# Performance work log

Hardware: AMD Instinct MI355X
Metric: run time of the kernel (lower is better)

The kernel has to match this reference:

```python
import jax, jax.numpy as jnp
import numpy as np

D_HEAD = 64
KERNEL = 7


def make_neighbourhood_mask(kernel: int, ch: int, cw: int) -> jnp.ndarray:
    """Boolean mask [ch*cw, ch*cw]; True where key is inside the query's k x k window."""
    h_ramp = jnp.arange(ch)
    w_ramp = jnp.arange(cw)
    h_pos, w_pos = jnp.meshgrid(h_ramp, w_ramp, indexing='ij')  # [ch, cw]
    start_h = jnp.clip(h_pos - kernel // 2, 0, ch - kernel)[..., None, None]
    end_h = start_h + kernel
    start_w = jnp.clip(w_pos - kernel // 2, 0, cw - kernel)[..., None, None]
    end_w = start_w + kernel
    h_range = h_ramp.reshape(1, 1, ch, 1)
    w_range = w_ramp.reshape(1, 1, 1, cw)
    mask = (h_range >= start_h) & (h_range < end_h) & (w_range >= start_w) & (w_range < end_w)
    return mask.reshape(ch * cw, ch * cw)


def setup_inputs() -> dict:
    key = jax.random.key(0)
    k1, k2, k3 = jax.random.split(key, 3)
    B, H, W, D = 2, 64, 64, 384
    x = jax.random.normal(k1, (B, H, W, D), dtype=jnp.float32)
    w_qkv = jax.random.normal(k2, (3 * D, D), dtype=jnp.float32) * 0.02
    w_out = jax.random.normal(k3, (D, D), dtype=jnp.float32) * 0.02
    return {"x": x, "w_qkv": w_qkv, "w_out": w_out}


def reference(x, w_qkv, w_out):
    B, H, W, D = x.shape
    nh = D // D_HEAD
    N = H * W
    # qkv projection: Linear(D, 3D, bias=False) -> x @ w_qkv.T
    qkv = jnp.einsum('bhwd,ed->bhwe', x, w_qkv)  # [B,H,W,3D]
    # 'n h w (t nh e) -> t n nh (h w) e'
    qkv = qkv.reshape(B, N, 3, nh, D_HEAD)
    qkv = jnp.transpose(qkv, (2, 0, 3, 1, 4))  # [3, B, nh, N, e]
    q, k, v = qkv[0], qkv[1], qkv[2]
    mask = make_neighbourhood_mask(KERNEL, H, W)  # [N, N] bool
    scale = 1.0 / jnp.sqrt(jnp.asarray(D_HEAD, dtype=x.dtype))
    scores = jnp.einsum('bnqe,bnke->bnqk', q, k) * scale  # [B,nh,N,N]
    neg = jnp.asarray(jnp.finfo(scores.dtype).min, dtype=scores.dtype)
    scores = jnp.where(mask[None, None], scores, neg)
    attn = jax.nn.softmax(scores, axis=-1)
    out = jnp.einsum('bnqk,bnke->bnqe', attn, v)  # [B,nh,N,e]
    # 'n nh (h w) e -> n h w (nh e)'
    out = jnp.transpose(out, (0, 2, 1, 3)).reshape(B, H, W, D)
    return jnp.einsum('bhwd,ed->bhwe', out, w_out)
```

## Files before the change

kernel.cpp:

```cpp
#include <hip/hip_runtime.h>
#include <hip/hip_bf16.h>

typedef __attribute__((ext_vector_type(8))) short bf16x8;
typedef __attribute__((ext_vector_type(4))) short s16x4;
typedef __attribute__((ext_vector_type(4))) float fx4;

#define MFMA16(a, b, c) __builtin_amdgcn_mfma_f32_16x16x32_bf16((a), (b), (c), 0, 0, 0)

__device__ __forceinline__ short f2bf(float f) {
  unsigned u = __float_as_uint(f);
  u += 0x7fffu + ((u >> 16) & 1u);
  return (short)(u >> 16);
}

__device__ __forceinline__ void gl_lds16(const short* g, short* l) {
  __builtin_amdgcn_global_load_lds((const __attribute__((address_space(1))) void*)(g),
                                   (__attribute__((address_space(3))) void*)(l), 16, 0, 0);
}

__global__ __launch_bounds__(256) void convert_k(
    const float* __restrict__ x, const float* __restrict__ wq, const float* __restrict__ wo,
    short* __restrict__ xb, short* __restrict__ wb, short* __restrict__ wob) {
  const int i4 = (blockIdx.x * 256 + threadIdx.x) * 4;
  {
    float4 v = *(const float4*)(x + i4);
    s16x4 s; s[0] = f2bf(v.x); s[1] = f2bf(v.y); s[2] = f2bf(v.z); s[3] = f2bf(v.w);
    *(s16x4*)(xb + i4) = s;
  }
  if (i4 < 1152 * 384) {
    float4 v = *(const float4*)(wq + i4);
    s16x4 s; s[0] = f2bf(v.x); s[1] = f2bf(v.y); s[2] = f2bf(v.z); s[3] = f2bf(v.w);
    *(s16x4*)(wb + i4) = s;
  }
  if (i4 < 384 * 384) {
    float4 v = *(const float4*)(wo + i4);
    s16x4 s; s[0] = f2bf(v.x); s[1] = f2bf(v.y); s[2] = f2bf(v.z); s[3] = f2bf(v.w);
    *(s16x4*)(wob + i4) = s;
  }
}

__global__ __launch_bounds__(256) void qkv_gemm(
    const short* __restrict__ A, const short* __restrict__ Bw,
    short* __restrict__ qb, short* __restrict__ kb, short* __restrict__ vb) {
  __shared__ __align__(16) short As[128 * 32];
  __shared__ __align__(16) short Bs[128 * 32];
  const int mt = blockIdx.x / 9, nt = blockIdx.x % 9;
  const int m0 = mt * 128, n0 = nt * 128;
  const int tid = threadIdx.x;
  const int lane = tid & 63, w = tid >> 6;
  const int wr = w >> 1, wc = w & 1;
  const int l15 = lane & 15, l4 = lane >> 4;
  const int srow = lane >> 2, schunk = (lane & 3) * 8;
  const fx4 vzero = {0.f, 0.f, 0.f, 0.f};
  fx4 acc[4][4];
#pragma unroll
  for (int i = 0; i < 4; i++)
#pragma unroll
    for (int j = 0; j < 4; j++) acc[i][j] = vzero;

  for (int kt = 0; kt < 384; kt += 32) {
    __syncthreads();
    gl_lds16(A + (size_t)(m0 + w * 16 + srow) * 384 + kt + schunk, As + (w * 16) * 32);
    gl_lds16(A + (size_t)(m0 + 64 + w * 16 + srow) * 384 + kt + schunk, As + (64 + w * 16) * 32);
    gl_lds16(Bw + (size_t)(n0 + w * 16 + srow) * 384 + kt + schunk, Bs + (w * 16) * 32);
    gl_lds16(Bw + (size_t)(n0 + 64 + w * 16 + srow) * 384 + kt + schunk, Bs + (64 + w * 16) * 32);
    __syncthreads();
    bf16x8 af[4], bfr[4];
#pragma unroll
    for (int i = 0; i < 4; i++) {
      af[i]  = *(const bf16x8*)(As + (wr * 64 + i * 16 + l15) * 32 + l4 * 8);
      bfr[i] = *(const bf16x8*)(Bs + (wc * 64 + i * 16 + l15) * 32 + l4 * 8);
    }
#pragma unroll
    for (int i = 0; i < 4; i++)
#pragma unroll
      for (int j = 0; j < 4; j++)
        acc[i][j] = MFMA16(af[i], bfr[j], acc[i][j]);
  }
#pragma unroll
  for (int j = 0; j < 4; j++) {
    const int e = n0 + wc * 64 + j * 16 + l15;
    const int t = e / 384;
    const int rem = e - t * 384;
    const int head = rem >> 6, d = rem & 63;
    short* __restrict__ dst = (t == 0) ? qb : (t == 1) ? kb : vb;
#pragma unroll
    for (int i = 0; i < 4; i++) {
      const int mb = m0 + wr * 64 + i * 16 + l4 * 4;
#pragma unroll
      for (int r = 0; r < 4; r++) {
        const int m = mb + r;
        const int b = m >> 12, pix = m & 4095;
        dst[((b * 6 + head) * 4096 + pix) * 64 + d] = f2bf(acc[i][j][r]);
      }
    }
  }
}

__global__ __launch_bounds__(256) void natt_k(
    const short* __restrict__ qg, const short* __restrict__ kg, const short* __restrict__ vg,
    short* __restrict__ ob) {
  __shared__ __align__(16) short lds[30976];
  short* Ks = lds;
  short* Vt = lds + 16128;
  short* Ps = lds;

  const int bid = blockIdx.x;
  const int tile = bid & 63, bh = bid >> 6;
  const int h0 = (tile >> 3) * 8, w0 = (tile & 7) * 8;
  const int ph0 = max(h0 - 3, 0), pw0 = max(w0 - 3, 0);
  const int prows = min(h0 + 4, 57) + 7 - ph0;
  const int pcols = min(w0 + 4, 57) + 7 - pw0;
  const short* kb = kg + (size_t)bh * 4096 * 64;
  const short* vb = vg + (size_t)bh * 4096 * 64;
  const short* qb = qg + (size_t)bh * 4096 * 64;
  const int tid = threadIdx.x;

  for (int i = tid; i < 224 * 8; i += 256) {
    const int kk = i >> 3, dc = i & 7;
    const int kr = kk >> 4, kc = kk & 15;
    const int krc = min(kr, prows - 1), kcc = min(kc, pcols - 1);
    const int pix = (ph0 + krc) * 64 + (pw0 + kcc);
    *(bf16x8*)(Ks + kk * 72 + dc * 8) = *(const bf16x8*)(kb + pix * 64 + dc * 8);
    const bf16x8 vv = *(const bf16x8*)(vb + pix * 64 + dc * 8);
#pragma unroll
    for (int j = 0; j < 8; j++) Vt[(dc * 8 + j) * 232 + kk] = vv[j];
  }
  __syncthreads();

  const int lane = tid & 63, w = tid >> 6;
  const int l15 = lane & 15, l4 = lane >> 4;

  const int qa = w * 16 + l15;
  const int qpixa = (h0 + (qa >> 3)) * 64 + (w0 + (qa & 7));
  const bf16x8 aq0 = *(const bf16x8*)(qb + qpixa * 64 + l4 * 8);
  const bf16x8 aq1 = *(const bf16x8*)(qb + qpixa * 64 + 32 + l4 * 8);

  const fx4 vzero = {0.f, 0.f, 0.f, 0.f};
  fx4 s[14];
#pragma unroll
  for (int n = 0; n < 14; n++) s[n] = vzero;
#pragma unroll
  for (int n = 0; n < 14; n++) {
    const bf16x8 b0 = *(const bf16x8*)(Ks + (n * 16 + l15) * 72 + l4 * 8);
    const bf16x8 b1 = *(const bf16x8*)(Ks + (n * 16 + l15) * 72 + 32 + l4 * 8);
    s[n] = MFMA16(aq0, b0, s[n]);
    s[n] = MFMA16(aq1, b1, s[n]);
  }

#pragma unroll
  for (int r = 0; r < 4; r++) {
    const int q = w * 16 + l4 * 4 + r;
    const int qh = h0 + (q >> 3), qw = w0 + (q & 7);
    const int sh = min(max(qh - 3, 0), 57) - ph0;
    const int sw = min(max(qw - 3, 0), 57) - pw0;
    float m = -1e30f;
#pragma unroll
    for (int n = 0; n < 14; n++) {
      const bool valid = (n >= sh) && (n < sh + 7) && (l15 >= sw) && (l15 < sw + 7);
      const float val = valid ? s[n][r] * 0.125f : -1e30f;
      s[n][r] = val;
      m = fmaxf(m, val);
    }
    m = fmaxf(m, __shfl_xor(m, 1));
    m = fmaxf(m, __shfl_xor(m, 2));
    m = fmaxf(m, __shfl_xor(m, 4));
    m = fmaxf(m, __shfl_xor(m, 8));
    float sum = 0.f;
#pragma unroll
    for (int n = 0; n < 14; n++) {
      const float e = __expf(s[n][r] - m);
      s[n][r] = e;
      sum += e;
    }
    sum += __shfl_xor(sum, 1);
    sum += __shfl_xor(sum, 2);
    sum += __shfl_xor(sum, 4);
    sum += __shfl_xor(sum, 8);
    const float inv = 1.f / sum;
#pragma unroll
    for (int n = 0; n < 14; n++) s[n][r] *= inv;
  }

  __syncthreads();

#pragma unroll
  for (int n = 0; n < 14; n++)
#pragma unroll
    for (int r = 0; r < 4; r++)
      Ps[(w * 16 + l4 * 4 + r) * 232 + n * 16 + l15] = f2bf(s[n][r]);

  __syncthreads();

  fx4 o[4];
#pragma unroll
  for (int j = 0; j < 4; j++) o[j] = vzero;
#pragma unroll
  for (int ks = 0; ks < 7; ks++) {
    const bf16x8 pa = *(const bf16x8*)(Ps + (w * 16 + l15) * 232 + ks * 32 + l4 * 8);
#pragma unroll
    for (int j = 0; j < 4; j++) {
      const bf16x8 vf = *(const bf16x8*)(Vt + (j * 16 + l15) * 232 + ks * 32 + l4 * 8);
      o[j] = MFMA16(pa, vf, o[j]);
    }
  }

  const int b = bh / 6, head = bh % 6;
#pragma unroll
  for (int j = 0; j < 4; j++) {
    const int d = j * 16 + l15;
#pragma unroll
    for (int r = 0; r < 4; r++) {
      const int q = w * 16 + l4 * 4 + r;
      const int pix = (h0 + (q >> 3)) * 64 + (w0 + (q & 7));
      ob[(size_t)(b * 4096 + pix) * 384 + head * 64 + d] = f2bf(o[j][r]);
    }
  }
}

__global__ __launch_bounds__(256) void out_gemm(
    const short* __restrict__ A, const short* __restrict__ Bw, float* __restrict__ out) {
  __shared__ __align__(16) short As[64 * 32];
  __shared__ __align__(16) short Bs[128 * 32];
  const int mt = blockIdx.x / 3, nt = blockIdx.x % 3;
  const int m0 = mt * 64, n0 = nt * 128;
  const int tid = threadIdx.x;
  const int lane = tid & 63, w = tid >> 6;
  const int wr = w >> 1, wc = w & 1;
  const int l15 = lane & 15, l4 = lane >> 4;
  const int srow = lane >> 2, schunk = (lane & 3) * 8;
  const fx4 vzero = {0.f, 0.f, 0.f, 0.f};
  fx4 acc[2][4];
#pragma unroll
  for (int i = 0; i < 2; i++)
#pragma unroll
    for (int j = 0; j < 4; j++) acc[i][j] = vzero;

  for (int kt = 0; kt < 384; kt += 32) {
    __syncthreads();
    gl_lds16(A + (size_t)(m0 + w * 16 + srow) * 384 + kt + schunk, As + (w * 16) * 32);
    gl_lds16(Bw + (size_t)(n0 + w * 16 + srow) * 384 + kt + schunk, Bs + (w * 16) * 32);
    gl_lds16(Bw + (size_t)(n0 + 64 + w * 16 + srow) * 384 + kt + schunk, Bs + (64 + w * 16) * 32);
    __syncthreads();
    bf16x8 af[2], bfr[4];
#pragma unroll
    for (int i = 0; i < 2; i++)
      af[i]  = *(const bf16x8*)(As + (wr * 32 + i * 16 + l15) * 32 + l4 * 8);
#pragma unroll
    for (int j = 0; j < 4; j++)
      bfr[j] = *(const bf16x8*)(Bs + (wc * 64 + j * 16 + l15) * 32 + l4 * 8);
#pragma unroll
    for (int i = 0; i < 2; i++)
#pragma unroll
      for (int j = 0; j < 4; j++)
        acc[i][j] = MFMA16(af[i], bfr[j], acc[i][j]);
  }
#pragma unroll
  for (int j = 0; j < 4; j++) {
    const int e = n0 + wc * 64 + j * 16 + l15;
#pragma unroll
    for (int i = 0; i < 2; i++) {
      const int mb = m0 + wr * 32 + i * 16 + l4 * 4;
#pragma unroll
      for (int r = 0; r < 4; r++)
        out[(size_t)(mb + r) * 384 + e] = acc[i][j][r];
    }
  }
}

extern "C" void kernel_launch(void* const* d_in, const int* in_sizes, int n_in,
                              void* d_out, int out_size, void* d_ws, size_t ws_size,
                              hipStream_t stream) {
  const float* x  = (const float*)d_in[0];
  const float* wq = (const float*)d_in[1];
  const float* wo = (const float*)d_in[2];
  float* out = (float*)d_out;

  short* xb  = (short*)d_ws;
  short* wb  = xb + 8192 * 384;
  short* wob = wb + 1152 * 384;
  short* qb  = wob + 384 * 384;
  short* kb  = qb + 3145728;
  short* vb  = kb + 3145728;
  short* ob  = vb + 3145728;

  convert_k<<<3072, 256, 0, stream>>>(x, wq, wo, xb, wb, wob);
  qkv_gemm<<<576, 256, 0, stream>>>(xb, wb, qb, kb, vb);
  natt_k<<<768, 256, 0, stream>>>(qb, kb, vb, ob);
  out_gemm<<<384, 256, 0, stream>>>(ob, wob, out);
}
```

Baseline: 54.97 us.

## Widen GEMM K-tile to 64 with XOR-swizzled LDS, remap blocks across XCDs, restructure V transpose

Both GEMMs now stage 64-wide K slices per iteration instead of 32, halving barrier and loop overhead. An XOR swizzle on the LDS column chunk avoids bank conflicts on fragment reads. Block indices in all three kernels are permuted so consecutive tiles land on the same XCD, which should improve L2 locality. The attention kernel's V transpose moves to one thread per key row looping over all chunks, which changes the LDS write pattern and leaves 32 threads idle.

```diff
diff --git a/kernel.cpp b/kernel.cpp
--- a/kernel.cpp
+++ b/kernel.cpp
@@ -42,15 +42,17 @@
 __global__ __launch_bounds__(256) void qkv_gemm(
     const short* __restrict__ A, const short* __restrict__ Bw,
     short* __restrict__ qb, short* __restrict__ kb, short* __restrict__ vb) {
-  __shared__ __align__(16) short As[128 * 32];
-  __shared__ __align__(16) short Bs[128 * 32];
-  const int mt = blockIdx.x / 9, nt = blockIdx.x % 9;
+  __shared__ __align__(16) short As[128 * 64];
+  __shared__ __align__(16) short Bs[128 * 64];
+  const int orig = (blockIdx.x & 7) * 72 + (blockIdx.x >> 3);
+  const int mt = orig / 9, nt = orig % 9;
   const int m0 = mt * 128, n0 = nt * 128;
   const int tid = threadIdx.x;
   const int lane = tid & 63, w = tid >> 6;
   const int wr = w >> 1, wc = w & 1;
   const int l15 = lane & 15, l4 = lane >> 4;
-  const int srow = lane >> 2, schunk = (lane & 3) * 8;
+  const int srow = lane >> 3;
+  const int scol = ((lane & 7) ^ (srow & 7)) * 8;
   const fx4 vzero = {0.f, 0.f, 0.f, 0.f};
   fx4 acc[4][4];
 #pragma unroll
@@ -58,24 +60,32 @@
 #pragma unroll
     for (int j = 0; j < 4; j++) acc[i][j] = vzero;
 
-  for (int kt = 0; kt < 384; kt += 32) {
+  for (int kt = 0; kt < 384; kt += 64) {
     __syncthreads();
-    gl_lds16(A + (size_t)(m0 + w * 16 + srow) * 384 + kt + schunk, As + (w * 16) * 32);
-    gl_lds16(A + (size_t)(m0 + 64 + w * 16 + srow) * 384 + kt + schunk, As + (64 + w * 16) * 32);
-    gl_lds16(Bw + (size_t)(n0 + w * 16 + srow) * 384 + kt + schunk, Bs + (w * 16) * 32);
-    gl_lds16(Bw + (size_t)(n0 + 64 + w * 16 + srow) * 384 + kt + schunk, Bs + (64 + w * 16) * 32);
+#pragma unroll
+    for (int q = 0; q < 4; q++) {
+      gl_lds16(A  + (size_t)(m0 + w * 32 + q * 8 + srow) * 384 + kt + scol, As + (w * 32 + q * 8) * 64);
+      gl_lds16(Bw + (size_t)(n0 + w * 32 + q * 8 + srow) * 384 + kt + scol, Bs + (w * 32 + q * 8) * 64);
+    }
     __syncthreads();
-    bf16x8 af[4], bfr[4];
+    bf16x8 af[4][2], bfr[4][2];
 #pragma unroll
     for (int i = 0; i < 4; i++) {
-      af[i]  = *(const bf16x8*)(As + (wr * 64 + i * 16 + l15) * 32 + l4 * 8);
-      bfr[i] = *(const bf16x8*)(Bs + (wc * 64 + i * 16 + l15) * 32 + l4 * 8);
+      const int ra = wr * 64 + i * 16 + l15;
+      const int rb = wc * 64 + i * 16 + l15;
+#pragma unroll
+      for (int kk = 0; kk < 2; kk++) {
+        af[i][kk]  = *(const bf16x8*)(As + ra * 64 + (((kk * 4 + l4) ^ (ra & 7)) * 8));
+        bfr[i][kk] = *(const bf16x8*)(Bs + rb * 64 + (((kk * 4 + l4) ^ (rb & 7)) * 8));
+      }
     }
 #pragma unroll
     for (int i = 0; i < 4; i++)
 #pragma unroll
-      for (int j = 0; j < 4; j++)
-        acc[i][j] = MFMA16(af[i], bfr[j], acc[i][j]);
+      for (int j = 0; j < 4; j++) {
+        acc[i][j] = MFMA16(af[i][0], bfr[j][0], acc[i][j]);
+        acc[i][j] = MFMA16(af[i][1], bfr[j][1], acc[i][j]);
+      }
   }
 #pragma unroll
   for (int j = 0; j < 4; j++) {
@@ -105,7 +115,7 @@
   short* Vt = lds + 16128;
   short* Ps = lds;
 
-  const int bid = blockIdx.x;
+  const int bid = (blockIdx.x & 7) * 96 + (blockIdx.x >> 3);
   const int tile = bid & 63, bh = bid >> 6;
   const int h0 = (tile >> 3) * 8, w0 = (tile & 7) * 8;
   const int ph0 = max(h0 - 3, 0), pw0 = max(w0 - 3, 0);
@@ -122,9 +132,18 @@
     const int krc = min(kr, prows - 1), kcc = min(kc, pcols - 1);
     const int pix = (ph0 + krc) * 64 + (pw0 + kcc);
     *(bf16x8*)(Ks + kk * 72 + dc * 8) = *(const bf16x8*)(kb + pix * 64 + dc * 8);
-    const bf16x8 vv = *(const bf16x8*)(vb + pix * 64 + dc * 8);
-#pragma unroll
-    for (int j = 0; j < 8; j++) Vt[(dc * 8 + j) * 232 + kk] = vv[j];
+  }
+  if (tid < 224) {
+    const int kk = tid;
+    const int kr = kk >> 4, kc = kk & 15;
+    const int krc = min(kr, prows - 1), kcc = min(kc, pcols - 1);
+    const int pix = (ph0 + krc) * 64 + (pw0 + kcc);
+#pragma unroll
+    for (int dc = 0; dc < 8; dc++) {
+      const bf16x8 vv = *(const bf16x8*)(vb + pix * 64 + dc * 8);
+#pragma unroll
+      for (int j = 0; j < 8; j++) Vt[(dc * 8 + j) * 232 + kk] = vv[j];
+    }
   }
   __syncthreads();
 
@@ -220,15 +239,17 @@
 
 __global__ __launch_bounds__(256) void out_gemm(
     const short* __restrict__ A, const short* __restrict__ Bw, float* __restrict__ out) {
-  __shared__ __align__(16) short As[64 * 32];
-  __shared__ __align__(16) short Bs[128 * 32];
-  const int mt = blockIdx.x / 3, nt = blockIdx.x % 3;
+  __shared__ __align__(16) short As[64 * 64];
+  __shared__ __align__(16) short Bs[128 * 64];
+  const int orig = (blockIdx.x & 7) * 48 + (blockIdx.x >> 3);
+  const int mt = orig / 3, nt = orig % 3;
   const int m0 = mt * 64, n0 = nt * 128;
   const int tid = threadIdx.x;
   const int lane = tid & 63, w = tid >> 6;
   const int wr = w >> 1, wc = w & 1;
   const int l15 = lane & 15, l4 = lane >> 4;
-  const int srow = lane >> 2, schunk = (lane & 3) * 8;
+  const int srow = lane >> 3;
+  const int scol = ((lane & 7) ^ (srow & 7)) * 8;
   const fx4 vzero = {0.f, 0.f, 0.f, 0.f};
   fx4 acc[2][4];
 #pragma unroll
@@ -236,24 +257,37 @@
 #pragma unroll
     for (int j = 0; j < 4; j++) acc[i][j] = vzero;
 
-  for (int kt = 0; kt < 384; kt += 32) {
+  for (int kt = 0; kt < 384; kt += 64) {
     __syncthreads();
-    gl_lds16(A + (size_t)(m0 + w * 16 + srow) * 384 + kt + schunk, As + (w * 16) * 32);
-    gl_lds16(Bw + (size_t)(n0 + w * 16 + srow) * 384 + kt + schunk, Bs + (w * 16) * 32);
-    gl_lds16(Bw + (size_t)(n0 + 64 + w * 16 + srow) * 384 + kt + schunk, Bs + (64 + w * 16) * 32);
+#pragma unroll
+    for (int q = 0; q < 2; q++)
+      gl_lds16(A + (size_t)(m0 + w * 16 + q * 8 + srow) * 384 + kt + scol, As + (w * 16 + q * 8) * 64);
+#pragma unroll
+    for (int q = 0; q < 4; q++)
+      gl_lds16(Bw + (size_t)(n0 + w * 32 + q * 8 + srow) * 384 + kt + scol, Bs + (w * 32 + q * 8) * 64);
     __syncthreads();
-    bf16x8 af[2], bfr[4];
+    bf16x8 af[2][2], bfr[4][2];
+#pragma unroll
+    for (int i = 0; i < 2; i++) {
+      const int ra = wr * 32 + i * 16 + l15;
+#pragma unroll
+      for (int kk = 0; kk < 2; kk++)
+        af[i][kk] = *(const bf16x8*)(As + ra * 64 + (((kk * 4 + l4) ^ (ra & 7)) * 8));
+    }
+#pragma unroll
+    for (int j = 0; j < 4; j++) {
+      const int rb = wc * 64 + j * 16 + l15;
+#pragma unroll
+      for (int kk = 0; kk < 2; kk++)
+        bfr[j][kk] = *(const bf16x8*)(Bs + rb * 64 + (((kk * 4 + l4) ^ (rb & 7)) * 8));
+    }
 #pragma unroll
     for (int i = 0; i < 2; i++)
-      af[i]  = *(const bf16x8*)(As + (wr * 32 + i * 16 + l15) * 32 + l4 * 8);
-#pragma unroll
-    for (int j = 0; j < 4; j++)
-      bfr[j] = *(const bf16x8*)(Bs + (wc * 64 + j * 16 + l15) * 32 + l4 * 8);
-#pragma unroll
-    for (int i = 0; i < 2; i++)
-#pragma unroll
-      for (int j = 0; j < 4; j++)
-        acc[i][j] = MFMA16(af[i], bfr[j], acc[i][j]);
+#pragma unroll
+      for (int j = 0; j < 4; j++) {
+        acc[i][j] = MFMA16(af[i][0], bfr[j][0], acc[i][j]);
+        acc[i][j] = MFMA16(af[i][1], bfr[j][1], acc[i][j]);
+      }
   }
 #pragma unroll
   for (int j = 0; j < 4; j++) {
```

New measurement: 51.62 us. 1.07x faster.
